# Performance work log

Hardware: AMD Instinct MI355X
Metric: run time of the kernel (lower is better)

## Reference

```python
import jax, jax.numpy as jnp
import numpy as np

B, E, IMG, PATCH, C, HEADS, DEPTH = 128, 512, 256, 32, 384, 3, 6
GRID = IMG // PATCH            # 8
NPATCH = GRID * GRID           # 64
N = NPATCH + 1                 # 65 tokens incl cls
HD = C // HEADS                # 128
MLP_H = 4 * C                  # 1536
SCALE = HD ** -0.5


def setup_inputs() -> dict:
    key = jax.random.key(0)
    ks = jax.random.split(key, 12)
    s = 0.02
    return {
        "images": jax.random.normal(ks[0], (B, 3, IMG, IMG), jnp.float32),
        "patch_w": jax.random.normal(ks[1], (C, 3, PATCH, PATCH), jnp.float32) * s,
        "patch_b": jnp.zeros((C,), jnp.float32),
        "cls_token": jax.random.normal(ks[2], (1, 1, C), jnp.float32) * s,
        "pos_embed": jax.random.normal(ks[3], (1, N, C), jnp.float32) * s,
        "norm1_w": jnp.ones((DEPTH, C), jnp.float32),
        "norm1_b": jnp.zeros((DEPTH, C), jnp.float32),
        "qkv_w": jax.random.normal(ks[4], (DEPTH, 3 * C, C), jnp.float32) * s,
        "proj_w": jax.random.normal(ks[5], (DEPTH, C, C), jnp.float32) * s,
        "proj_b": jnp.zeros((DEPTH, C), jnp.float32),
        "norm2_w": jnp.ones((DEPTH, C), jnp.float32),
        "norm2_b": jnp.zeros((DEPTH, C), jnp.float32),
        "fc1_w": jax.random.normal(ks[6], (DEPTH, MLP_H, C), jnp.float32) * s,
        "fc1_b": jnp.zeros((DEPTH, MLP_H), jnp.float32),
        "fc2_w": jax.random.normal(ks[7], (DEPTH, C, MLP_H), jnp.float32) * s,
        "fc2_b": jnp.zeros((DEPTH, C), jnp.float32),
        "norm_w": jnp.ones((C,), jnp.float32),
        "norm_b": jnp.zeros((C,), jnp.float32),
        "edge_index": jax.random.randint(ks[8], (2, E), 0, B, dtype=jnp.int32),
    }


def _ln(x, w, b):
    mu = x.mean(-1, keepdims=True)
    v = ((x - mu) ** 2).mean(-1, keepdims=True)
    return (x - mu) * jax.lax.rsqrt(v + 1e-5) * w + b


def _forward(images, patch_w, patch_b, cls_token, pos_embed,
             norm1_w, norm1_b, qkv_w, proj_w, proj_b,
             norm2_w, norm2_b, fc1_w, fc1_b, fc2_w, fc2_b,
             norm_w, norm_b, edge_index):
    src, dst = edge_index[0], edge_index[1]  # PyG: x_j = x[src], aggregate over dst
    cnt = jax.ops.segment_sum(jnp.ones((E,), jnp.float32), dst, num_segments=B)
    cnt = jnp.clip(cnt, 1.0)[:, None, None]  # scatter-mean denominator

    # PatchEmbed: conv stride = kernel = PATCH
    p = jax.lax.conv_general_dilated(images, patch_w, (PATCH, PATCH), 'VALID',
                                     dimension_numbers=('NCHW', 'OIHW', 'NCHW'))
    p = p + patch_b[None, :, None, None]
    p = p.reshape(B, C, NPATCH).transpose(0, 2, 1)          # [B, 64, C]
    x = jnp.concatenate([jnp.broadcast_to(cls_token, (B, 1, C)), p], axis=1) + pos_embed  # [B, N, C]

    for d in range(DEPTH):
        # MEConv2: LN -> qkv -> per-edge attention (q,v from target i; k from source j) -> proj -> scatter-mean
        y = _ln(x, norm1_w[d], norm1_b[d])
        qkv = (y @ qkv_w[d].T).reshape(B, N, 3, HEADS, HD)
        q = qkv[:, :, 0][dst]   # [E, N, H, HD]
        k = qkv[:, :, 1][src]
        v = qkv[:, :, 2][dst]
        attn = jnp.einsum('enhd,emhd->ehnm', q, k) * SCALE   # [E, H, N, N]
        a = jax.nn.softmax(attn, axis=-1)
        o = jnp.einsum('ehnm,emhd->enhd', a, v).reshape(E, N, C)
        msg = o @ proj_w[d].T + proj_b[d]                    # [E, N, C]
        agg = jax.ops.segment_sum(msg, dst, num_segments=B) / cnt
        x = x + agg
        # Block MLP residual
        h = _ln(x, norm2_w[d], norm2_b[d])
        h = jax.nn.gelu(h @ fc1_w[d].T + fc1_b[d], approximate=False)
        x = x + (h @ fc2_w[d].T + fc2_b[d])

    x = _ln(x, norm_w, norm_b)
    return x[:, 0]  # cls token features, [B, C]


def reference(images, patch_w, patch_b, cls_token, pos_embed,
              norm1_w, norm1_b, qkv_w, proj_w, proj_b,
              norm2_w, norm2_b, fc1_w, fc1_b, fc2_w, fc2_b,
              norm_w, norm_b, edge_index):
    return _forward(images, patch_w, patch_b, cls_token, pos_embed,
                    norm1_w, norm1_b, qkv_w, proj_w, proj_b,
                    norm2_w, norm2_b, fc1_w, fc1_b, fc2_w, fc2_b,
                    norm_w, norm_b, edge_index)
```

## Files before the change

kernel.cpp:

```cpp
#include <hip/hip_runtime.h>

typedef unsigned short u16;
typedef unsigned int   u32;
typedef __attribute__((ext_vector_type(4))) float f32x4;
using bf16x8 = __attribute__((ext_vector_type(8))) __bf16;

#define AS1 __attribute__((address_space(1)))
#define AS3 __attribute__((address_space(3)))

#define SCALE_ 0.08838834764831845f

#define X_OFF      0ull
#define Y_OFF      12779520ull
#define QKV_OFF    19169280ull
#define OBAR_OFF   38338560ull
#define SCR_OFF    44728320ull
#define PE_OFF     70287360ull
#define WB_OFF     95059968ull
#define ELIST_OFF  118652928ull
#define EOFF_OFF   118654976ull
#define INV_OFF    118655744ull
#define BSC_OFF    118656256ull
#define DLIST_OFF  118656768ull

#define PW_E   0
#define QW_E   1179648
#define PRW_E  3833856
#define F1W_E  4718592
#define F2W_E  8257536

__device__ __forceinline__ u16 f2bf(float f){
  union { float fv; u32 u; } x; x.fv = f;
  u32 r = x.u + 0x7FFFu + ((x.u >> 16) & 1u);
  return (u16)(r >> 16);
}
__device__ __forceinline__ float bf2f(u16 u){
  union { u32 u; float fv; } x; x.u = ((u32)u) << 16;
  return x.fv;
}
__device__ __forceinline__ void gld16(const void* g, void* l){
  __builtin_amdgcn_global_load_lds((AS1 void*)g, (AS3 void*)l, 16, 0, 0);
}

__global__ void cvt_k(const float* __restrict__ s, u16* __restrict__ d, int n4){
  int i = blockIdx.x*256 + threadIdx.x;
  if (i >= n4) return;
  float4 v = ((const float4*)s)[i];
  ushort4 o; o.x=f2bf(v.x); o.y=f2bf(v.y); o.z=f2bf(v.z); o.w=f2bf(v.w);
  ((ushort4*)d)[i] = o;
}

__global__ void im2col_k(const float* __restrict__ img, u16* __restrict__ A){
  int idx = blockIdx.x*256 + threadIdx.x;
  int m = idx / 384, k8 = idx - m*384;
  int k = k8 * 8;
  int c  = k >> 10;
  int kh = (k >> 5) & 31;
  int kw = k & 31;
  int b = m >> 6, p = m & 63;
  int ph = p >> 3, pw = p & 7;
  const float* src = img + ((size_t)(b*3 + c)*256 + ph*32 + kh)*256 + pw*32 + kw;
  float4 v0 = *(const float4*)src;
  float4 v1 = *(const float4*)(src + 4);
  uint4 ov; u16* tp = (u16*)&ov;
  tp[0]=f2bf(v0.x); tp[1]=f2bf(v0.y); tp[2]=f2bf(v0.z); tp[3]=f2bf(v0.w);
  tp[4]=f2bf(v1.x); tp[5]=f2bf(v1.y); tp[6]=f2bf(v1.z); tp[7]=f2bf(v1.w);
  *(uint4*)(A + (size_t)m*3072 + k) = ov;
}

__global__ void cls_init_k(const float* __restrict__ cls, const float* __restrict__ pos,
                           float* __restrict__ X){
  int idx = blockIdx.x*256 + threadIdx.x;
  int b = idx / 384, c = idx - b*384;
  X[(size_t)b*65*384 + c] = cls[c] + pos[c];
}

__global__ void edge_prep_k(const int* __restrict__ ei, int* __restrict__ elist,
                            int* __restrict__ eoff, float* __restrict__ inv,
                            float* __restrict__ bsc, int* __restrict__ dlist){
  __shared__ int cnt[128];
  __shared__ int off[129];
  int t = threadIdx.x;
  if (t < 128) cnt[t] = 0;
  __syncthreads();
  for (int e = t; e < 512; e += 256) atomicAdd(&cnt[ei[512 + e]], 1);
  __syncthreads();
  if (t == 0){
    off[0] = 0;
    for (int b = 0; b < 128; b++) off[b+1] = off[b] + cnt[b];
    for (int b = 0; b < 128; b++) cnt[b] = 0;
    for (int e = 0; e < 512; e++){
      int b = ei[512 + e];
      int pos = off[b] + cnt[b]++;
      elist[pos] = ei[e];
      dlist[pos] = b;
    }
    for (int b = 0; b < 129; b++) eoff[b] = off[b];
    for (int b = 0; b < 128; b++){
      int c = off[b+1] - off[b];
      inv[b] = 1.0f / (float)(c > 1 ? c : 1);
      bsc[b] = (c > 0) ? 1.0f : 0.0f;
    }
  }
}

__global__ __launch_bounds__(256) void ln_k(const float* __restrict__ X,
                                            const float* __restrict__ w,
                                            const float* __restrict__ b,
                                            u16* __restrict__ Y){
  int row  = blockIdx.x*4 + (threadIdx.x >> 6);
  int lane = threadIdx.x & 63;
  const float* xr = X + (size_t)row*384;
  float v[6]; float s = 0.f;
  #pragma unroll
  for (int i=0;i<6;i++){ v[i] = xr[lane + i*64]; s += v[i]; }
  #pragma unroll
  for (int m=1;m<64;m<<=1) s += __shfl_xor(s, m);
  float mu = s * (1.f/384.f);
  float q = 0.f;
  #pragma unroll
  for (int i=0;i<6;i++){ float d = v[i]-mu; q += d*d; }
  #pragma unroll
  for (int m=1;m<64;m<<=1) q += __shfl_xor(q, m);
  float rs = rsqrtf(q*(1.f/384.f) + 1e-5f);
  u16* yr = Y + (size_t)row*384;
  #pragma unroll
  for (int i=0;i<6;i++){ int e = lane + i*64; yr[e] = f2bf((v[i]-mu)*rs*w[e] + b[e]); }
}

__global__ __launch_bounds__(256) void ln_final_k(const float* __restrict__ X,
                                                  const float* __restrict__ w,
                                                  const float* __restrict__ b,
                                                  float* __restrict__ out){
  int bb   = blockIdx.x*4 + (threadIdx.x >> 6);
  int lane = threadIdx.x & 63;
  const float* xr = X + (size_t)bb*65*384;
  float v[6]; float s = 0.f;
  #pragma unroll
  for (int i=0;i<6;i++){ v[i] = xr[lane + i*64]; s += v[i]; }
  #pragma unroll
  for (int m=1;m<64;m<<=1) s += __shfl_xor(s, m);
  float mu = s * (1.f/384.f);
  float q = 0.f;
  #pragma unroll
  for (int i=0;i<6;i++){ float d = v[i]-mu; q += d*d; }
  #pragma unroll
  for (int m=1;m<64;m<<=1) q += __shfl_xor(q, m);
  float rs = rsqrtf(q*(1.f/384.f) + 1e-5f);
  #pragma unroll
  for (int i=0;i<6;i++){ int e = lane + i*64; out[(size_t)bb*384 + e] = (v[i]-mu)*rs*w[e] + b[e]; }
}

template<int MODE>
__global__ __launch_bounds__(256) void gemm_nt(
    const u16* __restrict__ A, const u16* __restrict__ W, int K,
    u16* __restrict__ outb, float* __restrict__ outf,
    const float* __restrict__ bias, const float* __restrict__ extra, int ldout)
{
  __shared__ u16 As[2][4096];
  __shared__ u16 Bs[2][8192];
  const int t    = threadIdx.x;
  const int lane = t & 63;
  const int w    = t >> 6;
  const int wr   = w >> 1, wc = w & 1;
  const int m0 = blockIdx.x * 64, n0 = blockIdx.y * 128;
  const int rs = t >> 3, cs = (t & 7) * 8;
  const u16* Ag = A + (size_t)(m0 + rs) * K + cs;
  const u16* Wg = W + (size_t)(n0 + rs) * K + cs;
  const size_t K32 = (size_t)K * 32;
  const int ln15 = lane & 15, l8 = (lane >> 4) * 8, lq = (lane >> 4) << 2;

  f32x4 acc[2][4] = {};
  const int nk = K >> 6;
  int cur = 0;

  gld16(Ag,           &As[0][t*8]);
  gld16(Ag + K32,     &As[0][2048 + t*8]);
  gld16(Wg,           &Bs[0][t*8]);
  gld16(Wg + K32,     &Bs[0][2048 + t*8]);
  gld16(Wg + 2*K32,   &Bs[0][4096 + t*8]);
  gld16(Wg + 3*K32,   &Bs[0][6144 + t*8]);
  __syncthreads();

  for (int kt = 1; kt <= nk; kt++){
    if (kt < nk){
      const int k0 = kt << 6;
      const int nb = cur ^ 1;
      gld16(Ag + k0,         &As[nb][t*8]);
      gld16(Ag + K32 + k0,   &As[nb][2048 + t*8]);
      gld16(Wg + k0,         &Bs[nb][t*8]);
      gld16(Wg + K32 + k0,   &Bs[nb][2048 + t*8]);
      gld16(Wg + 2*K32 + k0, &Bs[nb][4096 + t*8]);
      gld16(Wg + 3*K32 + k0, &Bs[nb][6144 + t*8]);
    }
    #pragma unroll
    for (int ks = 0; ks < 2; ks++){
      bf16x8 af[2], bfr[4];
      #pragma unroll
      for (int mi=0; mi<2; mi++)
        af[mi] = *(const bf16x8*)(&As[cur][(wr*32 + mi*16 + ln15)*64 + ks*32 + l8]);
      #pragma unroll
      for (int ni=0; ni<4; ni++)
        bfr[ni] = *(const bf16x8*)(&Bs[cur][(wc*64 + ni*16 + ln15)*64 + ks*32 + l8]);
      #pragma unroll
      for (int mi=0; mi<2; mi++)
        #pragma unroll
        for (int ni=0; ni<4; ni++)
          acc[mi][ni] = __builtin_amdgcn_mfma_f32_16x16x32_bf16(af[mi], bfr[ni], acc[mi][ni], 0,0,0);
    }
    if (kt < nk) __syncthreads();
    cur ^= 1;
  }

  #pragma unroll
  for (int mi=0; mi<2; mi++){
    #pragma unroll
    for (int j=0; j<4; j++){
      const int m = m0 + wr*32 + mi*16 + lq + j;
      #pragma unroll
      for (int ni=0; ni<4; ni++){
        const int n = n0 + wc*64 + ni*16 + ln15;
        float v = acc[mi][ni][j];
        if constexpr (MODE == 0){
          outb[(size_t)m*ldout + n] = f2bf(v);
        } else if constexpr (MODE == 1){
          int bb = m >> 6, p = m & 63;
          outf[((size_t)bb*65 + 1 + p)*384 + n] = v + bias[n] + extra[(1+p)*384 + n];
        } else if constexpr (MODE == 2){
          outf[(size_t)m*384 + n] += v + extra[m/65]*bias[n];
        } else if constexpr (MODE == 3){
          float g = v + bias[n];
          g = 0.5f*g*(1.f + erff(g*0.70710678118f));
          outb[(size_t)m*ldout + n] = f2bf(g);
        } else {
          outf[(size_t)m*384 + n] += v + bias[n];
        }
      }
    }
  }
}

__global__ __launch_bounds__(256) void qk_k(
    const u16* __restrict__ qkv, u16* __restrict__ Pe,
    const int* __restrict__ elist, const int* __restrict__ dlist)
{
  __shared__ u16 Qs[80*128];
  __shared__ u16 Ks[80*128];
  const int ee = blockIdx.x, h = blockIdx.y;
  const int t = threadIdx.x, w = t >> 6, lane = t & 63;
  const int ln15 = lane & 15, lq = (lane >> 4) << 2, l8 = (lane >> 4) * 8;
  const int b = dlist[ee], s = elist[ee];
  const size_t qbase = (size_t)b*65*1152 + h*128;
  const size_t kbase = (size_t)s*65*1152 + 384 + h*128;

  for (int idx = t; idx < 1040; idx += 256){
    int n = idx >> 4, cc = (idx & 15)*8;
    gld16(qkv + qbase + (size_t)n*1152 + cc, Qs + idx*8);
    gld16(qkv + kbase + (size_t)n*1152 + cc, Ks + idx*8);
  }
  __syncthreads();

  u16* pe = Pe + ((size_t)ee*3 + h)*6400;
  for (int rt = w; rt < 5; rt += 4){
    f32x4 sc[5] = {};
    #pragma unroll
    for (int ks=0; ks<4; ks++){
      bf16x8 a = *(const bf16x8*)(Qs + (rt*16 + ln15)*128 + ks*32 + l8);
      #pragma unroll
      for (int ct=0; ct<5; ct++){
        bf16x8 kb = *(const bf16x8*)(Ks + (ct*16 + ln15)*128 + ks*32 + l8);
        sc[ct] = __builtin_amdgcn_mfma_f32_16x16x32_bf16(a, kb, sc[ct], 0,0,0);
      }
    }
    #pragma unroll
    for (int j=0;j<4;j++){
      const int r = rt*16 + lq + j;
      const bool c4ok = (ln15 == 0);
      float ev[5];
      float mx = -1e30f;
      #pragma unroll
      for (int ct=0; ct<5; ct++){
        float sv = sc[ct][j] * SCALE_;
        ev[ct] = sv;
        if (ct < 4 || c4ok) mx = fmaxf(mx, sv);
      }
      #pragma unroll
      for (int mm=1; mm<16; mm<<=1) mx = fmaxf(mx, __shfl_xor(mx, mm));
      float se = 0.f;
      #pragma unroll
      for (int ct=0; ct<5; ct++){
        ev[ct] = (ct < 4 || c4ok) ? expf(ev[ct]-mx) : 0.f;
        se += ev[ct];
      }
      #pragma unroll
      for (int mm=1; mm<16; mm<<=1) se += __shfl_xor(se, mm);
      const float pscale = 1.f / se;
      #pragma unroll
      for (int ct=0; ct<5; ct++)
        pe[r*80 + ct*16 + ln15] = f2bf(ev[ct]*pscale);
    }
  }
}

__global__ __launch_bounds__(256) void pv_k(
    const u16* __restrict__ qkv, const u16* __restrict__ Pe,
    u16* __restrict__ obar, const int* __restrict__ eoff,
    const float* __restrict__ invc)
{
  __shared__ u16 Pb[80*96];
  __shared__ u16 Vt[128*96];
  const int b = blockIdx.x, h = blockIdx.y;
  const int t = threadIdx.x, w = t >> 6, lane = t & 63;
  const int ln15 = lane & 15, lq = (lane >> 4) << 2, l8 = (lane >> 4) * 8;
  const int e0 = eoff[b], e1 = eoff[b+1];
  const float inv = invc[b];

  float acc[25];
  #pragma unroll
  for (int i=0;i<25;i++) acc[i] = 0.f;
  for (int ee = e0; ee < e1; ee++){
    const u16* pe = Pe + ((size_t)ee*3 + h)*6400;
    #pragma unroll
    for (int i=0;i<25;i++) acc[i] += bf2f(pe[t + i*256]);
  }
  #pragma unroll
  for (int i=0;i<25;i++){
    int idx = t + i*256; int r = idx/80, c = idx - r*80;
    Pb[r*96 + c] = f2bf(acc[i]*inv);
  }
  for (int idx = t; idx < 80*16; idx += 256)
    Pb[(idx>>4)*96 + 80 + (idx & 15)] = 0;
  for (int idx = t; idx < 128*31; idx += 256){
    int d = idx / 31, m = 65 + (idx - d*31);
    Vt[d*96 + m] = 0;
  }
  const size_t vbase = (size_t)b*65*1152 + 768 + h*128;
  for (int idx = t; idx < 1040; idx += 256){
    int m = idx >> 4, dc = (idx & 15)*8;
    uint4 v = *(const uint4*)(qkv + vbase + (size_t)m*1152 + dc);
    const u16* p = (const u16*)&v;
    #pragma unroll
    for (int i=0;i<8;i++) Vt[(dc+i)*96 + m] = p[i];
  }
  __syncthreads();

  for (int ntile = w*2; ntile < w*2+2; ntile++){
    #pragma unroll
    for (int mt=0; mt<5; mt++){
      f32x4 oc = {};
      #pragma unroll
      for (int ks=0; ks<3; ks++){
        bf16x8 a  = *(const bf16x8*)(Pb + (mt*16 + ln15)*96 + ks*32 + l8);
        bf16x8 vb = *(const bf16x8*)(Vt + (ntile*16 + ln15)*96 + ks*32 + l8);
        oc = __builtin_amdgcn_mfma_f32_16x16x32_bf16(a, vb, oc, 0,0,0);
      }
      #pragma unroll
      for (int j=0;j<4;j++){
        int n = mt*16 + lq + j;
        if (n < 65) obar[((size_t)b*65 + n)*384 + h*128 + ntile*16 + ln15] = f2bf(oc[j]);
      }
    }
  }
}

extern "C" void kernel_launch(void* const* d_in, const int* in_sizes, int n_in,
                              void* d_out, int out_size, void* d_ws, size_t ws_size,
                              hipStream_t stream) {
  (void)in_sizes; (void)n_in; (void)out_size; (void)ws_size;
  const float* images  = (const float*)d_in[0];
  const float* patch_w = (const float*)d_in[1];
  const float* patch_b = (const float*)d_in[2];
  const float* cls_tok = (const float*)d_in[3];
  const float* pos_emb = (const float*)d_in[4];
  const float* n1w = (const float*)d_in[5];
  const float* n1b = (const float*)d_in[6];
  const float* qkvw = (const float*)d_in[7];
  const float* projw = (const float*)d_in[8];
  const float* projb = (const float*)d_in[9];
  const float* n2w = (const float*)d_in[10];
  const float* n2b = (const float*)d_in[11];
  const float* f1w = (const float*)d_in[12];
  const float* f1b = (const float*)d_in[13];
  const float* f2w = (const float*)d_in[14];
  const float* f2b = (const float*)d_in[15];
  const float* nw  = (const float*)d_in[16];
  const float* nb  = (const float*)d_in[17];
  const int*   eidx = (const int*)d_in[18];

  char* ws = (char*)d_ws;
  float* X   = (float*)(ws + X_OFF);
  u16*   Y   = (u16*)(ws + Y_OFF);
  u16*   QKV = (u16*)(ws + QKV_OFF);
  u16*   OB  = (u16*)(ws + OBAR_OFF);
  u16*   SCR = (u16*)(ws + SCR_OFF);
  u16*   PE  = (u16*)(ws + PE_OFF);
  u16*   WB  = (u16*)(ws + WB_OFF);
  int*   ELIST = (int*)(ws + ELIST_OFF);
  int*   EOFF  = (int*)(ws + EOFF_OFF);
  float* INV   = (float*)(ws + INV_OFF);
  float* BSC   = (float*)(ws + BSC_OFF);
  int*   DLIST = (int*)(ws + DLIST_OFF);

  cvt_k<<<1152, 256, 0, stream>>>(patch_w, WB + PW_E, 294912);
  cvt_k<<<2592, 256, 0, stream>>>(qkvw,    WB + QW_E, 663552);
  cvt_k<<<864,  256, 0, stream>>>(projw,   WB + PRW_E, 221184);
  cvt_k<<<3456, 256, 0, stream>>>(f1w,     WB + F1W_E, 884736);
  cvt_k<<<3456, 256, 0, stream>>>(f2w,     WB + F2W_E, 884736);

  edge_prep_k<<<1, 256, 0, stream>>>(eidx, ELIST, EOFF, INV, BSC, DLIST);
  im2col_k<<<12288, 256, 0, stream>>>(images, SCR);
  cls_init_k<<<192, 256, 0, stream>>>(cls_tok, pos_emb, X);

  gemm_nt<1><<<dim3(128, 3), 256, 0, stream>>>(SCR, WB + PW_E, 3072,
                                               nullptr, X, patch_b, pos_emb, 0);

  for (int d = 0; d < 6; d++){
    ln_k<<<2080, 256, 0, stream>>>(X, n1w + d*384, n1b + d*384, Y);
    gemm_nt<0><<<dim3(130, 9), 256, 0, stream>>>(Y, WB + QW_E + (size_t)d*1152*384, 384,
                                                 QKV, nullptr, nullptr, nullptr, 1152);
    qk_k<<<dim3(512, 3), 256, 0, stream>>>(QKV, PE, ELIST, DLIST);
    pv_k<<<dim3(128, 3), 256, 0, stream>>>(QKV, PE, OB, EOFF, INV);
    gemm_nt<2><<<dim3(130, 3), 256, 0, stream>>>(OB, WB + PRW_E + (size_t)d*384*384, 384,
                                                 nullptr, X, projb + d*384, BSC, 0);
    ln_k<<<2080, 256, 0, stream>>>(X, n2w + d*384, n2b + d*384, Y);
    gemm_nt<3><<<dim3(130, 12), 256, 0, stream>>>(Y, WB + F1W_E + (size_t)d*1536*384, 384,
                                                  SCR, nullptr, f1b + d*1536, nullptr, 1536);
    gemm_nt<4><<<dim3(130, 3), 256, 0, stream>>>(SCR, WB + F2W_E + (size_t)d*384*1536, 1536,
                                                 nullptr, X, f2b + d*384, nullptr, 0);
  }

  ln_final_k<<<32, 256, 0, stream>>>(X, nw, nb, (float*)d_out);
}
```

Measured before the change: 998.0 us.

## Merge weight conversions, parallelize edge prep, use five waves in qk kernel

Replaces the five weight-conversion launches with one combined kernel that selects the source by index range, cutting four launches. The edge preprocessing kernel loads edges into shared memory and lets each of 128 threads count and emit its own destination's edges, instead of a single serial thread. The qk attention kernel now runs 320 threads so each of the five row tiles gets its own wave, removing the second pass for wave 0, and guards writes to rows beyond 65. These remove launch and serial overheads, at the cost of some branch divergence in conversion and a larger block.

Measured after the change: 992.6 us. No clear change (-0.5%).

```diff
diff --git a/kernel.cpp b/kernel.cpp
--- a/kernel.cpp
+++ b/kernel.cpp
@@ -29,6 +29,12 @@
 #define F1W_E  4718592
 #define F2W_E  8257536
 
+#define R0_ 294912
+#define R1_ 958464
+#define R2_ 1179648
+#define R3_ 2064384
+#define R4_ 2949120
+
 __device__ __forceinline__ u16 f2bf(float f){
   union { float fv; u32 u; } x; x.fv = f;
   u32 r = x.u + 0x7FFFu + ((x.u >> 16) & 1u);
@@ -42,10 +48,17 @@
   __builtin_amdgcn_global_load_lds((AS1 void*)g, (AS3 void*)l, 16, 0, 0);
 }
 
-__global__ void cvt_k(const float* __restrict__ s, u16* __restrict__ d, int n4){
+__global__ void cvt_all_k(const float* __restrict__ s0, const float* __restrict__ s1,
+                          const float* __restrict__ s2, const float* __restrict__ s3,
+                          const float* __restrict__ s4, u16* __restrict__ d){
   int i = blockIdx.x*256 + threadIdx.x;
-  if (i >= n4) return;
-  float4 v = ((const float4*)s)[i];
+  const float* s; int rel;
+  if (i < R0_)      { s = s0; rel = i; }
+  else if (i < R1_) { s = s1; rel = i - R0_; }
+  else if (i < R2_) { s = s2; rel = i - R1_; }
+  else if (i < R3_) { s = s3; rel = i - R2_; }
+  else              { s = s4; rel = i - R3_; }
+  float4 v = ((const float4*)s)[rel];
   ushort4 o; o.x=f2bf(v.x); o.y=f2bf(v.y); o.z=f2bf(v.z); o.w=f2bf(v.w);
   ((ushort4*)d)[i] = o;
 }
@@ -75,32 +88,31 @@
   X[(size_t)b*65*384 + c] = cls[c] + pos[c];
 }
 
-__global__ void edge_prep_k(const int* __restrict__ ei, int* __restrict__ elist,
-                            int* __restrict__ eoff, float* __restrict__ inv,
-                            float* __restrict__ bsc, int* __restrict__ dlist){
+__global__ __launch_bounds__(128) void edge_prep_k(const int* __restrict__ ei,
+                                                   int* __restrict__ elist,
+                                                   int* __restrict__ eoff,
+                                                   float* __restrict__ inv,
+                                                   float* __restrict__ bsc,
+                                                   int* __restrict__ dlist){
+  __shared__ int srcS[512];
+  __shared__ int dstS[512];
   __shared__ int cnt[128];
-  __shared__ int off[129];
-  int t = threadIdx.x;
-  if (t < 128) cnt[t] = 0;
+  const int t = threadIdx.x;
+  for (int e = t; e < 512; e += 128){ srcS[e] = ei[e]; dstS[e] = ei[512 + e]; }
   __syncthreads();
-  for (int e = t; e < 512; e += 256) atomicAdd(&cnt[ei[512 + e]], 1);
+  int c = 0;
+  for (int e = 0; e < 512; e++) c += (dstS[e] == t) ? 1 : 0;
+  cnt[t] = c;
   __syncthreads();
-  if (t == 0){
-    off[0] = 0;
-    for (int b = 0; b < 128; b++) off[b+1] = off[b] + cnt[b];
-    for (int b = 0; b < 128; b++) cnt[b] = 0;
-    for (int e = 0; e < 512; e++){
-      int b = ei[512 + e];
-      int pos = off[b] + cnt[b]++;
-      elist[pos] = ei[e];
-      dlist[pos] = b;
-    }
-    for (int b = 0; b < 129; b++) eoff[b] = off[b];
-    for (int b = 0; b < 128; b++){
-      int c = off[b+1] - off[b];
-      inv[b] = 1.0f / (float)(c > 1 ? c : 1);
-      bsc[b] = (c > 0) ? 1.0f : 0.0f;
-    }
+  int off = 0;
+  for (int b = 0; b < t; b++) off += cnt[b];
+  eoff[t] = off;
+  if (t == 127) eoff[128] = off + c;
+  inv[t] = 1.0f / (float)(c > 1 ? c : 1);
+  bsc[t] = (c > 0) ? 1.0f : 0.0f;
+  int p = off;
+  for (int e = 0; e < 512; e++){
+    if (dstS[e] == t){ elist[p] = srcS[e]; dlist[p] = t; p++; }
   }
 }
 
@@ -240,7 +252,7 @@
   }
 }
 
-__global__ __launch_bounds__(256) void qk_k(
+__global__ __launch_bounds__(320) void qk_k(
     const u16* __restrict__ qkv, u16* __restrict__ Pe,
     const int* __restrict__ elist, const int* __restrict__ dlist)
 {
@@ -253,7 +265,7 @@
   const size_t qbase = (size_t)b*65*1152 + h*128;
   const size_t kbase = (size_t)s*65*1152 + 384 + h*128;
 
-  for (int idx = t; idx < 1040; idx += 256){
+  for (int idx = t; idx < 1040; idx += 320){
     int n = idx >> 4, cc = (idx & 15)*8;
     gld16(qkv + qbase + (size_t)n*1152 + cc, Qs + idx*8);
     gld16(qkv + kbase + (size_t)n*1152 + cc, Ks + idx*8);
@@ -261,7 +273,8 @@
   __syncthreads();
 
   u16* pe = Pe + ((size_t)ee*3 + h)*6400;
-  for (int rt = w; rt < 5; rt += 4){
+  {
+    const int rt = w;
     f32x4 sc[5] = {};
     #pragma unroll
     for (int ks=0; ks<4; ks++){
@@ -295,9 +308,11 @@
       #pragma unroll
       for (int mm=1; mm<16; mm<<=1) se += __shfl_xor(se, mm);
       const float pscale = 1.f / se;
-      #pragma unroll
-      for (int ct=0; ct<5; ct++)
-        pe[r*80 + ct*16 + ln15] = f2bf(ev[ct]*pscale);
+      if (r < 65){
+        #pragma unroll
+        for (int ct=0; ct<5; ct++)
+          pe[r*80 + ct*16 + ln15] = f2bf(ev[ct]*pscale);
+      }
     }
   }
 }
@@ -401,13 +416,9 @@
   float* BSC   = (float*)(ws + BSC_OFF);
   int*   DLIST = (int*)(ws + DLIST_OFF);
 
-  cvt_k<<<1152, 256, 0, stream>>>(patch_w, WB + PW_E, 294912);
-  cvt_k<<<2592, 256, 0, stream>>>(qkvw,    WB + QW_E, 663552);
-  cvt_k<<<864,  256, 0, stream>>>(projw,   WB + PRW_E, 221184);
-  cvt_k<<<3456, 256, 0, stream>>>(f1w,     WB + F1W_E, 884736);
-  cvt_k<<<3456, 256, 0, stream>>>(f2w,     WB + F2W_E, 884736);
-
-  edge_prep_k<<<1, 256, 0, stream>>>(eidx, ELIST, EOFF, INV, BSC, DLIST);
+  cvt_all_k<<<11520, 256, 0, stream>>>(patch_w, qkvw, projw, f1w, f2w, WB);
+
+  edge_prep_k<<<1, 128, 0, stream>>>(eidx, ELIST, EOFF, INV, BSC, DLIST);
   im2col_k<<<12288, 256, 0, stream>>>(images, SCR);
   cls_init_k<<<192, 256, 0, stream>>>(cls_tok, pos_emb, X);
 
@@ -418,7 +429,7 @@
     ln_k<<<2080, 256, 0, stream>>>(X, n1w + d*384, n1b + d*384, Y);
     gemm_nt<0><<<dim3(130, 9), 256, 0, stream>>>(Y, WB + QW_E + (size_t)d*1152*384, 384,
                                                  QKV, nullptr, nullptr, nullptr, 1152);
-    qk_k<<<dim3(512, 3), 256, 0, stream>>>(QKV, PE, ELIST, DLIST);
+    qk_k<<<dim3(512, 3), 320, 0, stream>>>(QKV, PE, ELIST, DLIST);
     pv_k<<<dim3(128, 3), 256, 0, stream>>>(QKV, PE, OB, EOFF, INV);
     gemm_nt<2><<<dim3(130, 3), 256, 0, stream>>>(OB, WB + PRW_E + (size_t)d*384*384, 384,
                                                  nullptr, X, projb + d*384, BSC, 0);
```
